# Kernel tuning notes

Hardware: AMD Instinct MI355X
Metric: run time of the kernel (lower is better)

The kernel has to match this reference:

```python
import jax, jax.numpy as jnp
import numpy as np

N_NODES = 50000
N_EDGES = 200000
D_FEAT = 512
D_HID = 1024


def setup_inputs() -> dict:
    key = jax.random.key(0)
    k_x, k_s, k_d, k_w1, k_w2 = jax.random.split(key, 5)
    x = jax.random.normal(k_x, (N_NODES, D_FEAT), dtype=jnp.float32)
    src = jax.random.randint(k_s, (N_EDGES,), 0, N_NODES, dtype=jnp.int64)
    dst = jax.random.randint(k_d, (N_EDGES,), 0, N_NODES, dtype=jnp.int64)
    # MLP params: Linear(2d -> hidden), ReLU, Linear(hidden -> 1)
    W1 = jax.random.normal(k_w1, (2 * D_FEAT, D_HID), dtype=jnp.float32) * (1.0 / np.sqrt(2 * D_FEAT))
    b1 = jnp.zeros((D_HID,), dtype=jnp.float32)
    W2 = jax.random.normal(k_w2, (D_HID, 1), dtype=jnp.float32) * (1.0 / np.sqrt(D_HID))
    b2 = jnp.zeros((1,), dtype=jnp.float32)
    return {"x": x, "src": src, "dst": dst, "W1": W1, "b1": b1, "W2": W2, "b2": b2}


def reference(x, src, dst, W1, b1, W2, b2):
    # Per-edge gather of src/dst node embeddings, concat along feature dim
    h = jnp.concatenate([x[src], x[dst]], axis=1)          # [E, 2d]
    h = jax.nn.relu(h @ W1 + b1)                            # [E, hidden]
    score = h @ W2 + b2                                     # [E, 1]
    return score
```

## Files before the change

kernel.cpp:

```cpp
#include <hip/hip_runtime.h>
#include <cstdint>
#include <cstddef>

typedef __attribute__((ext_vector_type(8))) short short8;
typedef __attribute__((ext_vector_type(4))) float f32x4;

#define D_FEAT 512
#define D_HID  1024
#define NCOL   2048

__device__ __forceinline__ unsigned short f2bf(float f) {
    unsigned u = __builtin_bit_cast(unsigned, f);
    u += 0x7FFFu + ((u >> 16) & 1u);
    return (unsigned short)(u >> 16);
}
__device__ __forceinline__ float bf2f(unsigned short h) {
    unsigned u = ((unsigned)h) << 16;
    return __builtin_bit_cast(float, u);
}

__global__ __launch_bounds__(256) void cast_x_kernel(const float* __restrict__ x,
                                                     unsigned short* __restrict__ xb,
                                                     int n) {
    int i = (blockIdx.x * 256 + threadIdx.x) * 8;
    if (i >= n) return;
    const float4* xp = (const float4*)(x + i);
    float4 a = xp[0], b = xp[1];
    short8 o;
    o[0] = (short)f2bf(a.x); o[1] = (short)f2bf(a.y);
    o[2] = (short)f2bf(a.z); o[3] = (short)f2bf(a.w);
    o[4] = (short)f2bf(b.x); o[5] = (short)f2bf(b.y);
    o[6] = (short)f2bf(b.z); o[7] = (short)f2bf(b.w);
    *(short8*)(xb + i) = o;
}

__global__ __launch_bounds__(256) void transpose_w1_kernel(const float* __restrict__ W1,
                                                           unsigned short* __restrict__ w1t) {
    __shared__ float tile[32][33];
    const int half = blockIdx.z;
    const int kb = blockIdx.y * 32;
    const int nb = blockIdx.x * 32;
    const int tx = threadIdx.x, ty = threadIdx.y;
    #pragma unroll
    for (int i = 0; i < 32; i += 8)
        tile[ty + i][tx] = W1[(size_t)(half * 512 + kb + ty + i) * 1024 + nb + tx];
    __syncthreads();
    #pragma unroll
    for (int i = 0; i < 32; i += 8)
        w1t[(size_t)(half * 1024 + nb + ty + i) * 512 + kb + tx] = f2bf(tile[tx][ty + i]);
}

#define BM 128
#define BN 128
#define BK 64

__global__ __launch_bounds__(256, 2) void gemm_uv_kernel(
    const unsigned short* __restrict__ xb,
    const unsigned short* __restrict__ w1t,
    const float* __restrict__ b1,
    unsigned short* __restrict__ UV,
    int M)
{
    __shared__ __align__(16) unsigned short smem[20480];
    unsigned short* sA = smem;
    unsigned short* sB = smem + 8192;

    const int tid  = threadIdx.x;
    const int wave = tid >> 6;
    const int lane = tid & 63;
    const int q    = lane >> 4;
    const int l15  = lane & 15;
    const int wm   = (wave >> 1) * 64;
    const int wn   = (wave & 1) * 64;
    const int m0   = blockIdx.x * BM;
    const int n0   = blockIdx.y * BN;

    const int ar = lane >> 3;
    const int ac = ((lane & 7) ^ ar) * 8;

    const int swz = l15 & 7;
    const int c0 = (q ^ swz) * 8;
    const int c1 = ((q ^ swz) ^ 4) * 8;

    f32x4 zero = {0.f, 0.f, 0.f, 0.f};
    f32x4 acc[4][4];
    #pragma unroll
    for (int i = 0; i < 4; ++i)
        #pragma unroll
        for (int j = 0; j < 4; ++j)
            acc[i][j] = zero;

    #pragma unroll 1
    for (int kt = 0; kt < 8; ++kt) {
        const int k0 = kt * BK;
        __syncthreads();
        #pragma unroll
        for (int i = 0; i < 4; ++i) {
            int slot = wave * 4 + i;
            int row  = slot * 8 + ar;
            int m    = m0 + row; if (m >= M) m = M - 1;
            __builtin_amdgcn_global_load_lds(
                (const __attribute__((address_space(1))) void*)(xb + (size_t)m * D_FEAT + k0 + ac),
                (__attribute__((address_space(3))) void*)(sA + slot * 512),
                16, 0, 0);
        }
        #pragma unroll
        for (int i = 0; i < 4; ++i) {
            int slot = wave * 4 + i;
            int row  = slot * 8 + ar;
            __builtin_amdgcn_global_load_lds(
                (const __attribute__((address_space(1))) void*)(w1t + (size_t)(n0 + row) * D_FEAT + k0 + ac),
                (__attribute__((address_space(3))) void*)(sB + slot * 512),
                16, 0, 0);
        }
        __syncthreads();
        {
            short8 a[4], b[4];
            #pragma unroll
            for (int mt = 0; mt < 4; ++mt)
                a[mt] = *(const short8*)(sA + (wm + mt * 16 + l15) * 64 + c0);
            #pragma unroll
            for (int nt = 0; nt < 4; ++nt)
                b[nt] = *(const short8*)(sB + (wn + nt * 16 + l15) * 64 + c0);
            #pragma unroll
            for (int mt = 0; mt < 4; ++mt)
                #pragma unroll
                for (int nt = 0; nt < 4; ++nt)
                    acc[mt][nt] = __builtin_amdgcn_mfma_f32_16x16x32_bf16(a[mt], b[nt], acc[mt][nt], 0, 0, 0);
            #pragma unroll
            for (int mt = 0; mt < 4; ++mt)
                a[mt] = *(const short8*)(sA + (wm + mt * 16 + l15) * 64 + c1);
            #pragma unroll
            for (int nt = 0; nt < 4; ++nt)
                b[nt] = *(const short8*)(sB + (wn + nt * 16 + l15) * 64 + c1);
            #pragma unroll
            for (int mt = 0; mt < 4; ++mt)
                #pragma unroll
                for (int nt = 0; nt < 4; ++nt)
                    acc[mt][nt] = __builtin_amdgcn_mfma_f32_16x16x32_bf16(a[mt], b[nt], acc[mt][nt], 0, 0, 0);
        }
    }

    float b1v[4];
    #pragma unroll
    for (int nt = 0; nt < 4; ++nt) {
        int n = n0 + wn + nt * 16 + l15;
        b1v[nt] = (n < D_HID) ? b1[n] : 0.f;
    }
    __syncthreads();
    unsigned short* ep = smem + wave * 5120;
    #pragma unroll
    for (int mt = 0; mt < 4; ++mt)
        #pragma unroll
        for (int nt = 0; nt < 4; ++nt)
            #pragma unroll
            for (int r = 0; r < 4; ++r) {
                float v = acc[mt][nt][r] + b1v[nt];
                ep[(mt * 16 + q * 4 + r) * 80 + nt * 16 + l15] = f2bf(v);
            }
    __syncthreads();
    #pragma unroll
    for (int i = 0; i < 8; ++i) {
        int flat = i * 64 + lane;
        int r  = flat >> 3;
        int c8 = (flat & 7) * 8;
        int m  = m0 + wm + r;
        if (m < M) {
            short8 v = *(const short8*)(ep + r * 80 + c8);
            *(short8*)(UV + (size_t)m * NCOL + n0 + wn + c8) = v;
        }
    }
}

__global__ __launch_bounds__(256) void edge_score_kernel(
    const unsigned short* __restrict__ UV,
    const int* __restrict__ src, const int* __restrict__ dst,
    const float* __restrict__ W2, const float* __restrict__ b2,
    float* __restrict__ out, int E)
{
    const int wave = threadIdx.x >> 6;
    const int lane = threadIdx.x & 63;
    const int e = blockIdx.x * 4 + wave;
    if (e >= E) return;
    const int s = src[e];
    const int d = dst[e];
    const unsigned short* up = UV + (size_t)s * NCOL + lane * 16;
    const unsigned short* vp = UV + (size_t)d * NCOL + D_HID + lane * 16;
    short8 u0 = *(const short8*)up;
    short8 u1 = *(const short8*)(up + 8);
    short8 v0 = *(const short8*)vp;
    short8 v1 = *(const short8*)(vp + 8);
    const float4* wp = (const float4*)(W2 + lane * 16);
    float4 wa = wp[0], wb = wp[1], wc = wp[2], wd = wp[3];
    float w[16] = {wa.x, wa.y, wa.z, wa.w, wb.x, wb.y, wb.z, wb.w,
                   wc.x, wc.y, wc.z, wc.w, wd.x, wd.y, wd.z, wd.w};
    float acc = 0.f;
    #pragma unroll
    for (int i = 0; i < 8; ++i) {
        float h = bf2f((unsigned short)u0[i]) + bf2f((unsigned short)v0[i]);
        acc = fmaf(fmaxf(h, 0.f), w[i], acc);
    }
    #pragma unroll
    for (int i = 0; i < 8; ++i) {
        float h = bf2f((unsigned short)u1[i]) + bf2f((unsigned short)v1[i]);
        acc = fmaf(fmaxf(h, 0.f), w[8 + i], acc);
    }
    #pragma unroll
    for (int off = 1; off < 64; off <<= 1)
        acc += __shfl_xor(acc, off);
    if (lane == 0) out[e] = acc + b2[0];
}

extern "C" void kernel_launch(void* const* d_in, const int* in_sizes, int n_in,
                              void* d_out, int out_size, void* d_ws, size_t ws_size,
                              hipStream_t stream) {
    const float* x  = (const float*)d_in[0];
    const int*   src = (const int*)d_in[1];
    const int*   dst = (const int*)d_in[2];
    const float* W1 = (const float*)d_in[3];
    const float* b1 = (const float*)d_in[4];
    const float* W2 = (const float*)d_in[5];
    const float* b2 = (const float*)d_in[6];
    float* out = (float*)d_out;

    const int M = in_sizes[0] / D_FEAT;
    const int E = in_sizes[1];

    char* ws = (char*)d_ws;
    unsigned short* UV  = (unsigned short*)ws;
    unsigned short* xb  = (unsigned short*)(ws + (size_t)M * NCOL * 2);
    unsigned short* w1t = (unsigned short*)(ws + (size_t)M * NCOL * 2 + (size_t)M * D_FEAT * 2);

    const int nx = M * D_FEAT;
    cast_x_kernel<<<(nx / 8 + 255) / 256, 256, 0, stream>>>(x, xb, nx);
    transpose_w1_kernel<<<dim3(32, 16, 2), dim3(32, 8), 0, stream>>>(W1, w1t);
    gemm_uv_kernel<<<dim3((M + BM - 1) / BM, NCOL / BN), 256, 0, stream>>>(xb, w1t, b1, UV, M);
    edge_score_kernel<<<(E + 3) / 4, 256, 0, stream>>>(UV, src, dst, W2, b2, out, E);
}
```

Baseline: 412.3 us.

## Bucket-sort edges by source node block to improve UV gather locality

Adds a counting sort of edges into buckets of 64 source nodes (zero histogram, atomic histogram, single-block scan, atomic scatter) that yields a permutation. The edge scoring kernel then visits edges in that order, so nearby waves read U rows from nearby nodes and get better L2 reuse. The cost is four extra small launches and atomics, plus a scattered write to out. Destination reads stay random.

```diff
diff --git a/kernel.cpp b/kernel.cpp
--- a/kernel.cpp
+++ b/kernel.cpp
@@ -8,6 +8,7 @@
 #define D_FEAT 512
 #define D_HID  1024
 #define NCOL   2048
+#define NBUCK  1024
 
 __device__ __forceinline__ unsigned short f2bf(float f) {
     unsigned u = __builtin_bit_cast(unsigned, f);
@@ -172,16 +173,55 @@
     }
 }
 
+__global__ __launch_bounds__(1024) void zero_hist_kernel(int* __restrict__ hist) {
+    hist[threadIdx.x] = 0;
+}
+
+__global__ __launch_bounds__(256) void hist_kernel(const int* __restrict__ src,
+                                                   int* __restrict__ hist, int E) {
+    int e = blockIdx.x * 256 + threadIdx.x;
+    if (e < E) atomicAdd(&hist[src[e] >> 6], 1);
+}
+
+__global__ __launch_bounds__(1024) void scan_kernel(const int* __restrict__ hist,
+                                                    int* __restrict__ off) {
+    __shared__ int tmp[NBUCK];
+    int t = threadIdx.x;
+    int v = hist[t];
+    tmp[t] = v;
+    __syncthreads();
+    #pragma unroll
+    for (int d = 1; d < NBUCK; d <<= 1) {
+        int add = (t >= d) ? tmp[t - d] : 0;
+        __syncthreads();
+        tmp[t] += add;
+        __syncthreads();
+    }
+    off[t] = tmp[t] - v;
+}
+
+__global__ __launch_bounds__(256) void scatter_kernel(const int* __restrict__ src,
+                                                      int* __restrict__ off,
+                                                      int* __restrict__ perm, int E) {
+    int e = blockIdx.x * 256 + threadIdx.x;
+    if (e < E) {
+        int pos = atomicAdd(&off[src[e] >> 6], 1);
+        perm[pos] = e;
+    }
+}
+
 __global__ __launch_bounds__(256) void edge_score_kernel(
     const unsigned short* __restrict__ UV,
+    const int* __restrict__ perm,
     const int* __restrict__ src, const int* __restrict__ dst,
     const float* __restrict__ W2, const float* __restrict__ b2,
     float* __restrict__ out, int E)
 {
     const int wave = threadIdx.x >> 6;
     const int lane = threadIdx.x & 63;
-    const int e = blockIdx.x * 4 + wave;
-    if (e >= E) return;
+    const int i = blockIdx.x * 4 + wave;
+    if (i >= E) return;
+    const int e = perm[i];
     const int s = src[e];
     const int d = dst[e];
     const unsigned short* up = UV + (size_t)s * NCOL + lane * 16;
@@ -196,14 +236,14 @@
                    wc.x, wc.y, wc.z, wc.w, wd.x, wd.y, wd.z, wd.w};
     float acc = 0.f;
     #pragma unroll
-    for (int i = 0; i < 8; ++i) {
-        float h = bf2f((unsigned short)u0[i]) + bf2f((unsigned short)v0[i]);
-        acc = fmaf(fmaxf(h, 0.f), w[i], acc);
-    }
-    #pragma unroll
-    for (int i = 0; i < 8; ++i) {
-        float h = bf2f((unsigned short)u1[i]) + bf2f((unsigned short)v1[i]);
-        acc = fmaf(fmaxf(h, 0.f), w[8 + i], acc);
+    for (int k = 0; k < 8; ++k) {
+        float h = bf2f((unsigned short)u0[k]) + bf2f((unsigned short)v0[k]);
+        acc = fmaf(fmaxf(h, 0.f), w[k], acc);
+    }
+    #pragma unroll
+    for (int k = 0; k < 8; ++k) {
+        float h = bf2f((unsigned short)u1[k]) + bf2f((unsigned short)v1[k]);
+        acc = fmaf(fmaxf(h, 0.f), w[8 + k], acc);
     }
     #pragma unroll
     for (int off = 1; off < 64; off <<= 1)
@@ -214,13 +254,13 @@
 extern "C" void kernel_launch(void* const* d_in, const int* in_sizes, int n_in,
                               void* d_out, int out_size, void* d_ws, size_t ws_size,
                               hipStream_t stream) {
-    const float* x  = (const float*)d_in[0];
+    const float* x   = (const float*)d_in[0];
     const int*   src = (const int*)d_in[1];
     const int*   dst = (const int*)d_in[2];
-    const float* W1 = (const float*)d_in[3];
-    const float* b1 = (const float*)d_in[4];
-    const float* W2 = (const float*)d_in[5];
-    const float* b2 = (const float*)d_in[6];
+    const float* W1  = (const float*)d_in[3];
+    const float* b1  = (const float*)d_in[4];
+    const float* W2  = (const float*)d_in[5];
+    const float* b2  = (const float*)d_in[6];
     float* out = (float*)d_out;
 
     const int M = in_sizes[0] / D_FEAT;
@@ -230,10 +270,19 @@
     unsigned short* UV  = (unsigned short*)ws;
     unsigned short* xb  = (unsigned short*)(ws + (size_t)M * NCOL * 2);
     unsigned short* w1t = (unsigned short*)(ws + (size_t)M * NCOL * 2 + (size_t)M * D_FEAT * 2);
+    char* p = ws + (size_t)M * NCOL * 2 + (size_t)M * D_FEAT * 2 + (size_t)NCOL * D_FEAT * 2;
+    int* hist = (int*)p;
+    int* off  = (int*)(p + NBUCK * 4);
+    int* perm = (int*)(p + 2 * NBUCK * 4);
 
     const int nx = M * D_FEAT;
+    zero_hist_kernel<<<1, NBUCK, 0, stream>>>(hist);
+    hist_kernel<<<(E + 255) / 256, 256, 0, stream>>>(src, hist, E);
+    scan_kernel<<<1, NBUCK, 0, stream>>>(hist, off);
+    scatter_kernel<<<(E + 255) / 256, 256, 0, stream>>>(src, off, perm, E);
+
     cast_x_kernel<<<(nx / 8 + 255) / 256, 256, 0, stream>>>(x, xb, nx);
     transpose_w1_kernel<<<dim3(32, 16, 2), dim3(32, 8), 0, stream>>>(W1, w1t);
     gemm_uv_kernel<<<dim3((M + BM - 1) / BM, NCOL / BN), 256, 0, stream>>>(xb, w1t, b1, UV, M);
-    edge_score_kernel<<<(E + 3) / 4, 256, 0, stream>>>(UV, src, dst, W2, b2, out, E);
-}
+    edge_score_kernel<<<(E + 3) / 4, 256, 0, stream>>>(UV, perm, src, dst, W2, b2, out, E);
+}
```

Result: slower. 514.9 us (+24.9%).
